# Kernel tuning notes

Measured on AMD Instinct MI355X. Metric: run time of the kernel, lower is better.

The kernel has to match this reference:

```python
import jax, jax.numpy as jnp
import numpy as np

B, S, D_IN, D_OUT = 4, 2048, 1024, 1024

def setup_inputs() -> dict:
    key = jax.random.key(0)
    k1, k2, k3, k4 = jax.random.split(key, 4)
    sc = 0.02
    return {
        "x": jax.random.normal(k1, (B, S, D_IN), dtype=jnp.float32),
        "Wq": jax.random.normal(k2, (D_OUT, D_IN), dtype=jnp.float32) * sc,
        "Wk": jax.random.normal(k3, (D_OUT, D_IN), dtype=jnp.float32) * sc,
        "Wv": jax.random.normal(k4, (D_OUT, D_IN), dtype=jnp.float32) * sc,
    }

def reference(x, Wq, Wk, Wv):
    # torch Linear: y = x @ W.T  (weights stored [out, in])
    b, n, _ = x.shape
    q = jnp.einsum('bnd,od->bno', x, Wq)  # [B,S,D_OUT]
    k = jnp.einsum('bnd,od->bno', x, Wk)
    v = jnp.einsum('bnd,od->bno', x, Wv)
    scores = jnp.einsum('bqd,bkd->bqk', q, k)  # [B,S,S]
    # causal mask: positions j > i masked to -inf BEFORE scaling (matches source)
    causal = jnp.triu(jnp.ones((n, n), dtype=bool), k=1)
    scores = jnp.where(causal[None, :, :], -jnp.inf, scores)
    scale = 1.0 / jnp.sqrt(jnp.float32(k.shape[-1]))
    attn = jax.nn.softmax(scores * scale, axis=-1)
    # NOTE: source calls dropout but discards its output -> no-op
    return jnp.einsum('bqk,bkd->bqd', attn, v)
```

## Files before the change

### kernel.cpp

```cpp
#include <hip/hip_runtime.h>
#include <hip/hip_bf16.h>


using bf16 = __hip_bfloat16;
typedef __bf16 bf16x8 __attribute__((ext_vector_type(8)));
typedef float f32x4 __attribute__((ext_vector_type(4)));

__device__ __forceinline__ void load_lds_16B(const void* g, void* l) {
  __builtin_amdgcn_global_load_lds(
      (const __attribute__((address_space(1))) unsigned int*)g,
      (__attribute__((address_space(3))) unsigned int*)l, 16, 0, 0);
}

template <int N>
__device__ __forceinline__ void waitcnt_vm() {
  if constexpr (N == 6) asm volatile("s_waitcnt vmcnt(6)" ::: "memory");
  else if constexpr (N == 5) asm volatile("s_waitcnt vmcnt(5)" ::: "memory");
  else asm volatile("s_waitcnt vmcnt(0)" ::: "memory");
}

__device__ __forceinline__ int swz(int o) { return o ^ (((o >> 7) & 7) << 4); }

template <int M_REP, bool OUT_BF16, bool CSKIP, bool KLIM>
__global__ __launch_bounds__(512, 2) void gemm8p(
    const bf16* __restrict__ A, const bf16* __restrict__ Bm, void* __restrict__ Cv,
    int M, int N, int K, long sAz, long sBz, long sCzBytes) {
  constexpr int BM = M_REP * 32, BN = 256;
  constexpr int MH2 = M_REP / 2;
  constexpr int AKC = BM * 64;
  constexpr int BKC = BN * 64;
  constexpr int DBSTR = 2 * AKC + 2 * BKC;
  constexpr int ACALLS = AKC / 8192;
  constexpr int VM_LEAVE = ACALLS + 4;

  const int tn = blockIdx.x, tm = blockIdx.y, z = blockIdx.z;
  if (CSKIP && tn > tm) return;
  A += (long)z * sAz;
  Bm += (long)z * sBz;
  char* C = (char*)Cv + (long)z * sCzBytes;

  int kEnd = K;
  if (KLIM) kEnd = min(tm * BM + BM, K);
  const int nt = kEnd >> 6;
  const int NI = nt >> 1;

  __shared__ __align__(128) char sm[2 * DBSTR];
  const int tid = threadIdx.x, lane = tid & 63, wv = tid >> 6;
  const int wr = wv >> 2, wc = wv & 3;
  const int ldsw = wv * 1024;

  const char* srcA[ACALLS];
  const char* srcB[2];
#pragma unroll
  for (int c = 0; c < ACALLS; c++) {
    int os = swz(c * 8192 + tid * 16);
    srcA[c] = (const char*)(A + ((long)tm * BM + (os >> 6)) * K) + (os & 63);
  }
#pragma unroll
  for (int c = 0; c < 2; c++) {
    int os = swz(c * 8192 + tid * 16);
    srcB[c] = (const char*)(Bm + ((long)tn * BN + (os >> 6)) * K) + (os & 63);
  }
  auto stageA = [&](int t, int kc) {
#pragma unroll
    for (int c = 0; c < ACALLS; c++)
      load_lds_16B(srcA[c] + (long)t * 128 + kc * 64,
                   sm + (t & 1) * DBSTR + kc * AKC + c * 8192 + ldsw);
  };
  auto stageB = [&](int t, int kc) {
#pragma unroll
    for (int c = 0; c < 2; c++)
      load_lds_16B(srcB[c] + (long)t * 128 + kc * 64,
                   sm + (t & 1) * DBSTR + 2 * AKC + kc * BKC + c * 8192 + ldsw);
  };

  int aoff[M_REP], boff[4];
#pragma unroll
  for (int m = 0; m < M_REP; m++)
    aoff[m] = swz((wr * (M_REP * 16) + m * 16 + (lane & 15)) * 64 + (lane >> 4) * 16);
#pragma unroll
  for (int n = 0; n < 4; n++)
    boff[n] = 2 * AKC + swz((wc * 64 + n * 16 + (lane & 15)) * 64 + (lane >> 4) * 16);

  f32x4 acc[M_REP][4] = {};
  bf16x8 bfr[2][4];
  bf16x8 afrA[MH2], afrB[MH2];

#define LDB(DBUF, KC)                                                          \
  _Pragma("unroll") for (int n = 0; n < 4; n++)                                \
      bfr[KC][n] = *(const bf16x8*)(sm + (DBUF)*DBSTR + (KC)*BKC + boff[n]);
#define LDA(DBUF, KC, MH, DST)                                                 \
  _Pragma("unroll") for (int m = 0; m < MH2; m++)                              \
      DST[m] = *(const bf16x8*)(sm + (DBUF)*DBSTR + (KC)*AKC + aoff[(MH)*MH2 + m]);
#define MFMAS(KC, MH, AFR)                                                     \
  __builtin_amdgcn_s_setprio(1);                                               \
  _Pragma("unroll") for (int m = 0; m < MH2; m++)                              \
      _Pragma("unroll") for (int n = 0; n < 4; n++)                            \
          acc[(MH)*MH2 + m][n] = __builtin_amdgcn_mfma_f32_16x16x32_bf16(      \
              AFR[m], bfr[KC][n], acc[(MH)*MH2 + m][n], 0, 0, 0);              \
  __builtin_amdgcn_s_setprio(0);
#define BAR1()                                                                 \
  __builtin_amdgcn_s_barrier();                                                \
  asm volatile("s_waitcnt lgkmcnt(0)" ::: "memory");                           \
  __builtin_amdgcn_sched_barrier(0);
#define BAR2() __builtin_amdgcn_s_barrier();

  stageB(0, 0); stageA(0, 0); stageB(0, 1); stageA(0, 1);
  stageB(1, 0); stageA(1, 0); stageB(1, 1);
  waitcnt_vm<VM_LEAVE>();
  __builtin_amdgcn_s_barrier();

  for (int i = 0; i < NI - 1; i++) {
    const int ta = 2 * i, tb = 2 * i + 1;
    LDB(0, 0); LDA(0, 0, 0, afrA); stageA(tb, 1);     BAR1(); MFMAS(0, 0, afrA); BAR2();
    LDA(0, 0, 1, afrB);            stageB(ta + 2, 0); BAR1(); MFMAS(0, 1, afrB); BAR2();
    LDB(0, 1); LDA(0, 1, 0, afrA); stageA(ta + 2, 0); BAR1(); MFMAS(1, 0, afrA); BAR2();
    LDA(0, 1, 1, afrB);            stageB(ta + 2, 1);
    waitcnt_vm<VM_LEAVE>();                           BAR1(); MFMAS(1, 1, afrB); BAR2();
    LDB(1, 0); LDA(1, 0, 0, afrA); stageA(ta + 2, 1); BAR1(); MFMAS(0, 0, afrA); BAR2();
    LDA(1, 0, 1, afrB);            stageB(tb + 2, 0); BAR1(); MFMAS(0, 1, afrB); BAR2();
    LDB(1, 1); LDA(1, 1, 0, afrA); stageA(tb + 2, 0); BAR1(); MFMAS(1, 0, afrA); BAR2();
    LDA(1, 1, 1, afrB);            stageB(tb + 2, 1);
    waitcnt_vm<VM_LEAVE>();                           BAR1(); MFMAS(1, 1, afrB); BAR2();
  }
  {
    const int tb = nt - 1;
    LDB(0, 0); LDA(0, 0, 0, afrA); stageA(tb, 1); BAR1(); MFMAS(0, 0, afrA); BAR2();
    LDA(0, 0, 1, afrB);                           BAR1(); MFMAS(0, 1, afrB); BAR2();
    LDB(0, 1); LDA(0, 1, 0, afrA);                BAR1(); MFMAS(1, 0, afrA); BAR2();
    LDA(0, 1, 1, afrB); waitcnt_vm<0>();          BAR1(); MFMAS(1, 1, afrB); BAR2();
    LDB(1, 0); LDA(1, 0, 0, afrA);                BAR1(); MFMAS(0, 0, afrA); BAR2();
    LDA(1, 0, 1, afrB);                           BAR1(); MFMAS(0, 1, afrB); BAR2();
    LDB(1, 1); LDA(1, 1, 0, afrA);                BAR1(); MFMAS(1, 0, afrA); BAR2();
    LDA(1, 1, 1, afrB);                           BAR1(); MFMAS(1, 1, afrB); BAR2();
  }
#undef LDB
#undef LDA
#undef MFMAS
#undef BAR1
#undef BAR2

  const int cr0 = tm * BM + wr * (M_REP * 16) + (lane >> 4) * 4;
  const int cc0 = tn * BN + wc * 64 + (lane & 15);
#pragma unroll
  for (int m = 0; m < M_REP; m++)
#pragma unroll
    for (int n = 0; n < 4; n++)
#pragma unroll
      for (int j = 0; j < 4; j++) {
        long row = cr0 + m * 16 + j;
        long col = cc0 + n * 16;
        if (OUT_BF16)
          ((bf16*)C)[row * (long)N + col] = __float2bfloat16(acc[m][n][j]);
        else
          ((float*)C)[row * (long)N + col] = acc[m][n][j];
      }
}

__global__ __launch_bounds__(256) void cvt_all(const float* __restrict__ x,
                                               const float* __restrict__ wq,
                                               const float* __restrict__ wk,
                                               const float* __restrict__ wv,
                                               bf16* __restrict__ xb,
                                               bf16* __restrict__ wb) {
  const int b = blockIdx.x;
  const float* src;
  bf16* dst;
  int i;
  if (b < 8192) { src = x; dst = xb; i = b * 256 + threadIdx.x; }
  else if (b < 9216) { src = wq; dst = wb; i = (b - 8192) * 256 + threadIdx.x; }
  else if (b < 10240) { src = wk; dst = wb + 1048576; i = (b - 9216) * 256 + threadIdx.x; }
  else { src = wv; dst = wb + 2097152; i = (b - 10240) * 256 + threadIdx.x; }
  float4 f = ((const float4*)src)[i];
  union { bf16 h[4]; uint2 u; } o;
  o.h[0] = __float2bfloat16(f.x);
  o.h[1] = __float2bfloat16(f.y);
  o.h[2] = __float2bfloat16(f.z);
  o.h[3] = __float2bfloat16(f.w);
  ((uint2*)dst)[i] = o.u;
}

__global__ __launch_bounds__(256) void softmax_causal(const float* __restrict__ Sc,
                                                      bf16* __restrict__ P) {
  const int i = blockIdx.x, b = blockIdx.y;
  const long base = ((long)b * 2048 + i) * 2048;
  const float4* row4 = (const float4*)(Sc + base);
  bf16* prow = P + base;
  const int tid = threadIdx.x, lane = tid & 63, wv = tid >> 6;
  const int len = i + 1;

  float v[8];
  float m = -3.3e38f;
#pragma unroll
  for (int u = 0; u < 2; u++) {
    float4 f = row4[tid + u * 256];
    int j0 = (tid + u * 256) * 4;
    float* pv = v + u * 4;
    pv[0] = f.x; pv[1] = f.y; pv[2] = f.z; pv[3] = f.w;
#pragma unroll
    for (int e = 0; e < 4; e++) {
      if (j0 + e >= len) pv[e] = -3.3e38f;
      m = fmaxf(m, pv[e]);
    }
  }
  for (int o = 32; o; o >>= 1) m = fmaxf(m, __shfl_xor(m, o));
  __shared__ float redm[4], reds[4];
  if (lane == 0) redm[wv] = m;
  __syncthreads();
  m = fmaxf(fmaxf(redm[0], redm[1]), fmaxf(redm[2], redm[3]));

  const float scale = 0.03125f;
  float e8[8];
  float s = 0.f;
#pragma unroll
  for (int u = 0; u < 2; u++) {
    int j0 = (tid + u * 256) * 4;
#pragma unroll
    for (int e = 0; e < 4; e++) {
      float t = (j0 + e < len) ? __expf((v[u * 4 + e] - m) * scale) : 0.f;
      e8[u * 4 + e] = t;
      s += t;
    }
  }
  for (int o = 32; o; o >>= 1) s += __shfl_xor(s, o);
  if (lane == 0) reds[wv] = s;
  __syncthreads();
  s = reds[0] + reds[1] + reds[2] + reds[3];
  const float inv = 1.0f / s;
#pragma unroll
  for (int u = 0; u < 2; u++) {
    int j0 = (tid + u * 256) * 4;
    union { bf16 h[4]; uint2 u2; } o;
#pragma unroll
    for (int e = 0; e < 4; e++) o.h[e] = __float2bfloat16(e8[u * 4 + e] * inv);
    *(uint2*)(prow + j0) = o.u2;
  }
}

__global__ __launch_bounds__(256) void transposeV(const bf16* __restrict__ V,
                                                  bf16* __restrict__ Vt) {
  __shared__ bf16 t[32][33];
  const int b = blockIdx.z;
  const int s0 = blockIdx.x << 5;
  const int d0 = blockIdx.y << 5;
  const bf16* Vb = V + (long)b * 2048 * 1024;
  bf16* Vtb = Vt + (long)b * 1024 * 2048;
  const int lx = threadIdx.x & 31, ly = threadIdx.x >> 5;
#pragma unroll
  for (int r = 0; r < 32; r += 8)
    t[r + ly][lx] = Vb[(long)(s0 + r + ly) * 1024 + d0 + lx];
  __syncthreads();
#pragma unroll
  for (int r = 0; r < 32; r += 8)
    Vtb[(long)(d0 + r + ly) * 2048 + s0 + lx] = t[lx][r + ly];
}

extern "C" void kernel_launch(void* const* d_in, const int* in_sizes, int n_in,
                              void* d_out, int out_size, void* d_ws, size_t ws_size,
                              hipStream_t stream) {
  const float* x = (const float*)d_in[0];
  const float* Wq = (const float*)d_in[1];
  const float* Wk = (const float*)d_in[2];
  const float* Wv = (const float*)d_in[3];

  const long MBy = 1 << 20;
  char* ws = (char*)d_ws;
  bf16* Q = (bf16*)(ws);
  bf16* Kb = (bf16*)(ws + 16 * MBy);
  bf16* V = (bf16*)(ws + 32 * MBy);
  bf16* Vt = (bf16*)(ws + 48 * MBy);
  bf16* P = (bf16*)(ws + 64 * MBy);
  float* Sc = (float*)(ws + 96 * MBy);
  bf16* xb = (bf16*)(ws + 96 * MBy);
  bf16* Wb = (bf16*)(ws + 112 * MBy);

  cvt_all<<<11264, 256, 0, stream>>>(x, Wq, Wk, Wv, xb, Wb);

  gemm8p<8, true, false, false><<<dim3(4, 32, 3), 512, 0, stream>>>(
      xb, Wb, Q, 8192, 1024, 1024, 0L, 1048576L, 16 * MBy);

  transposeV<<<dim3(64, 32, 4), 256, 0, stream>>>(V, Vt);

  gemm8p<8, false, true, false><<<dim3(8, 8, 4), 512, 0, stream>>>(
      Q, Kb, Sc, 2048, 2048, 1024, 2048L * 1024, 2048L * 1024, 2048L * 2048 * 4);

  softmax_causal<<<dim3(2048, 4), 256, 0, stream>>>(Sc, P);

  gemm8p<4, false, false, true><<<dim3(4, 16, 4), 512, 0, stream>>>(
      P, Vt, d_out, 2048, 1024, 2048, 2048L * 2048, 1024L * 2048, 2048L * 1024 * 4);
}
```

Before: 169.4 us.

## Fuse QKV projection into one GEMM and store scores in fp16

Replaces the z-batched QKV projection with a single GEMM over concatenated weights, writing an interleaved [tokens, 3*D] buffer read through leading-dimension strides. The score matrix is written as fp16 rather than fp32, and softmax reads it with 16-byte vector loads and writes P with 16-byte stores. This halves the score write/read traffic and reshapes the projection tiling. The risk is fp16 range or precision loss on the unscaled scores, plus a smaller M tile in the projection GEMM.

```diff
diff --git a/kernel.cpp b/kernel.cpp
--- a/kernel.cpp
+++ b/kernel.cpp
@@ -1,5 +1,6 @@
 #include <hip/hip_runtime.h>
 #include <hip/hip_bf16.h>
+#include <hip/hip_fp16.h>
 
 
 using bf16 = __hip_bfloat16;
@@ -21,10 +22,10 @@
 
 __device__ __forceinline__ int swz(int o) { return o ^ (((o >> 7) & 7) << 4); }
 
-template <int M_REP, bool OUT_BF16, bool CSKIP, bool KLIM>
+template <int M_REP, int OUT, bool CSKIP, bool KLIM>
 __global__ __launch_bounds__(512, 2) void gemm8p(
     const bf16* __restrict__ A, const bf16* __restrict__ Bm, void* __restrict__ Cv,
-    int M, int N, int K, long sAz, long sBz, long sCzBytes) {
+    int K, int lda, int ldb, int ldc, long sAz, long sBz, long sCzBytes) {
   constexpr int BM = M_REP * 32, BN = 256;
   constexpr int MH2 = M_REP / 2;
   constexpr int AKC = BM * 64;
@@ -54,12 +55,12 @@
 #pragma unroll
   for (int c = 0; c < ACALLS; c++) {
     int os = swz(c * 8192 + tid * 16);
-    srcA[c] = (const char*)(A + ((long)tm * BM + (os >> 6)) * K) + (os & 63);
+    srcA[c] = (const char*)(A + ((long)tm * BM + (os >> 6)) * lda) + (os & 63);
   }
 #pragma unroll
   for (int c = 0; c < 2; c++) {
     int os = swz(c * 8192 + tid * 16);
-    srcB[c] = (const char*)(Bm + ((long)tn * BN + (os >> 6)) * K) + (os & 63);
+    srcB[c] = (const char*)(Bm + ((long)tn * BN + (os >> 6)) * ldb) + (os & 63);
   }
   auto stageA = [&](int t, int kc) {
 #pragma unroll
@@ -150,10 +151,12 @@
       for (int j = 0; j < 4; j++) {
         long row = cr0 + m * 16 + j;
         long col = cc0 + n * 16;
-        if (OUT_BF16)
-          ((bf16*)C)[row * (long)N + col] = __float2bfloat16(acc[m][n][j]);
+        if (OUT == 1)
+          ((bf16*)C)[row * (long)ldc + col] = __float2bfloat16(acc[m][n][j]);
+        else if (OUT == 2)
+          ((__half*)C)[row * (long)ldc + col] = __float2half(acc[m][n][j]);
         else
-          ((float*)C)[row * (long)N + col] = acc[m][n][j];
+          ((float*)C)[row * (long)ldc + col] = acc[m][n][j];
       }
 }
 
@@ -180,27 +183,29 @@
   ((uint2*)dst)[i] = o.u;
 }
 
-__global__ __launch_bounds__(256) void softmax_causal(const float* __restrict__ Sc,
+typedef short short4v __attribute__((ext_vector_type(4)));
+
+__global__ __launch_bounds__(256) void softmax_causal(const __half* __restrict__ Sc,
                                                       bf16* __restrict__ P) {
   const int i = blockIdx.x, b = blockIdx.y;
   const long base = ((long)b * 2048 + i) * 2048;
-  const float4* row4 = (const float4*)(Sc + base);
+  const __half* row = Sc + base;
   bf16* prow = P + base;
   const int tid = threadIdx.x, lane = tid & 63, wv = tid >> 6;
   const int len = i + 1;
 
   float v[8];
   float m = -3.3e38f;
-#pragma unroll
-  for (int u = 0; u < 2; u++) {
-    float4 f = row4[tid + u * 256];
-    int j0 = (tid + u * 256) * 4;
-    float* pv = v + u * 4;
-    pv[0] = f.x; pv[1] = f.y; pv[2] = f.z; pv[3] = f.w;
-#pragma unroll
-    for (int e = 0; e < 4; e++) {
-      if (j0 + e >= len) pv[e] = -3.3e38f;
-      m = fmaxf(m, pv[e]);
+  {
+    const int j0 = tid * 8;
+    union { short4v s[2]; __half h[8]; } u;
+    u.s[0] = *(const short4v*)(row + j0);
+    u.s[1] = *(const short4v*)(row + j0 + 4);
+#pragma unroll
+    for (int e = 0; e < 8; e++) {
+      float t = __half2float(u.h[e]);
+      v[e] = (j0 + e < len) ? t : -3.3e38f;
+      m = fmaxf(m, v[e]);
     }
   }
   for (int o = 32; o; o >>= 1) m = fmaxf(m, __shfl_xor(m, o));
@@ -212,13 +217,12 @@
   const float scale = 0.03125f;
   float e8[8];
   float s = 0.f;
-#pragma unroll
-  for (int u = 0; u < 2; u++) {
-    int j0 = (tid + u * 256) * 4;
-#pragma unroll
-    for (int e = 0; e < 4; e++) {
-      float t = (j0 + e < len) ? __expf((v[u * 4 + e] - m) * scale) : 0.f;
-      e8[u * 4 + e] = t;
+  {
+    const int j0 = tid * 8;
+#pragma unroll
+    for (int e = 0; e < 8; e++) {
+      float t = (j0 + e < len) ? __expf((v[e] - m) * scale) : 0.f;
+      e8[e] = t;
       s += t;
     }
   }
@@ -227,13 +231,12 @@
   __syncthreads();
   s = reds[0] + reds[1] + reds[2] + reds[3];
   const float inv = 1.0f / s;
-#pragma unroll
-  for (int u = 0; u < 2; u++) {
-    int j0 = (tid + u * 256) * 4;
-    union { bf16 h[4]; uint2 u2; } o;
-#pragma unroll
-    for (int e = 0; e < 4; e++) o.h[e] = __float2bfloat16(e8[u * 4 + e] * inv);
-    *(uint2*)(prow + j0) = o.u2;
+  {
+    const int j0 = tid * 8;
+    union { bf16 h[8]; uint4 u4; } o;
+#pragma unroll
+    for (int e = 0; e < 8; e++) o.h[e] = __float2bfloat16(e8[e] * inv);
+    *(uint4*)(prow + j0) = o.u4;
   }
 }
 
@@ -243,12 +246,12 @@
   const int b = blockIdx.z;
   const int s0 = blockIdx.x << 5;
   const int d0 = blockIdx.y << 5;
-  const bf16* Vb = V + (long)b * 2048 * 1024;
+  const bf16* Vb = V + (long)b * 2048 * 3072;
   bf16* Vtb = Vt + (long)b * 1024 * 2048;
   const int lx = threadIdx.x & 31, ly = threadIdx.x >> 5;
 #pragma unroll
   for (int r = 0; r < 32; r += 8)
-    t[r + ly][lx] = Vb[(long)(s0 + r + ly) * 1024 + d0 + lx];
+    t[r + ly][lx] = Vb[(long)(s0 + r + ly) * 3072 + d0 + lx];
   __syncthreads();
 #pragma unroll
   for (int r = 0; r < 32; r += 8)
@@ -265,27 +268,27 @@
 
   const long MBy = 1 << 20;
   char* ws = (char*)d_ws;
-  bf16* Q = (bf16*)(ws);
-  bf16* Kb = (bf16*)(ws + 16 * MBy);
-  bf16* V = (bf16*)(ws + 32 * MBy);
+  bf16* Cqkv = (bf16*)(ws);
   bf16* Vt = (bf16*)(ws + 48 * MBy);
   bf16* P = (bf16*)(ws + 64 * MBy);
-  float* Sc = (float*)(ws + 96 * MBy);
+  __half* Sc = (__half*)(ws + 96 * MBy);
   bf16* xb = (bf16*)(ws + 96 * MBy);
   bf16* Wb = (bf16*)(ws + 112 * MBy);
 
   cvt_all<<<11264, 256, 0, stream>>>(x, Wq, Wk, Wv, xb, Wb);
 
-  gemm8p<8, true, false, false><<<dim3(4, 32, 3), 512, 0, stream>>>(
-      xb, Wb, Q, 8192, 1024, 1024, 0L, 1048576L, 16 * MBy);
-
-  transposeV<<<dim3(64, 32, 4), 256, 0, stream>>>(V, Vt);
-
-  gemm8p<8, false, true, false><<<dim3(8, 8, 4), 512, 0, stream>>>(
-      Q, Kb, Sc, 2048, 2048, 1024, 2048L * 1024, 2048L * 1024, 2048L * 2048 * 4);
+  gemm8p<4, 1, false, false><<<dim3(12, 64), 512, 0, stream>>>(
+      xb, Wb, Cqkv, 1024, 1024, 1024, 3072, 0L, 0L, 0L);
+
+  transposeV<<<dim3(64, 32, 4), 256, 0, stream>>>(Cqkv + 2048, Vt);
+
+  gemm8p<8, 2, true, false><<<dim3(8, 8, 4), 512, 0, stream>>>(
+      Cqkv, Cqkv + 1024, Sc, 1024, 3072, 3072, 2048,
+      2048L * 3072, 2048L * 3072, 2048L * 2048 * 2);
 
   softmax_causal<<<dim3(2048, 4), 256, 0, stream>>>(Sc, P);
 
-  gemm8p<4, false, false, true><<<dim3(4, 16, 4), 512, 0, stream>>>(
-      P, Vt, d_out, 2048, 1024, 2048, 2048L * 2048, 1024L * 2048, 2048L * 1024 * 4);
-}
+  gemm8p<4, 0, false, true><<<dim3(4, 16, 4), 512, 0, stream>>>(
+      P, Vt, d_out, 2048, 2048, 2048, 1024,
+      2048L * 2048, 1024L * 2048, 2048L * 1024 * 4);
+}
```

Result: no change. 169.4 us (+0.0%).
